# Performance work log

Measured on AMD Instinct MI355X. Metric: run time of the kernel, lower is better.

## Reference

```python
import jax, jax.numpy as jnp
import numpy as np

B, L, H, E = 2, 2048, 16, 64  # self-attention: S=L, D=E


def setup_inputs() -> dict:
    key = jax.random.key(0)
    kq, kk, kv = jax.random.split(key, 3)
    queries = jax.random.normal(kq, (B, L, H, E), dtype=jnp.float32)
    keys = jax.random.normal(kk, (B, L, H, E), dtype=jnp.float32)
    values = jax.random.normal(kv, (B, L, H, E), dtype=jnp.float32)
    return {"queries": queries, "keys": keys, "values": values}


def reference(queries, keys, values):
    # Faithful to source: scale is computed in torch code but never applied.
    # scores: [B, H, L, S]
    scores = jnp.einsum("blhe,bshe->bhls", queries, keys)
    # TriangularCausalMask: triu(ones, diagonal=1) -> mask strictly-future positions
    Lq = queries.shape[1]
    causal = jnp.triu(jnp.ones((Lq, Lq), dtype=bool), k=1)  # [L, S]
    scores = jnp.where(causal[None, None, :, :], -jnp.inf, scores)
    A = jax.nn.softmax(scores, axis=-1)  # dropout in eval mode = identity
    V = jnp.einsum("bhls,bshd->blhd", A, values)
    return V
```

## Files before the change

### kernel.cpp

```cpp
#include <hip/hip_runtime.h>

typedef short bf16x8 __attribute__((ext_vector_type(8)));
typedef short bf16x4 __attribute__((ext_vector_type(4)));
typedef short bf16x2 __attribute__((ext_vector_type(2)));
typedef float f32x4 __attribute__((ext_vector_type(4)));

#define LOG2E 1.4426950408889634f

static __device__ __forceinline__ unsigned short f2bf(float x) {
  unsigned int u = __builtin_bit_cast(unsigned int, x);
  u += 0x7fffu + ((u >> 16) & 1u);
  return (unsigned short)(u >> 16);
}
static __device__ __forceinline__ float bf2f(unsigned short h) {
  unsigned int u = ((unsigned int)h) << 16;
  return __builtin_bit_cast(float, u);
}

static __device__ __forceinline__ void gl_lds16(const void* g, void* l) {
  __builtin_amdgcn_global_load_lds(
      (const __attribute__((address_space(1))) void*)g,
      (__attribute__((address_space(3))) void*)l, 16, 0, 0);
}

__global__ __launch_bounds__(256)
void prep_kv(const float* __restrict__ K, const float* __restrict__ V,
             short* __restrict__ ws) {
  __shared__ float tmp[64 * 65];
  const int isV = blockIdx.x >> 10;
  const int tile = blockIdx.x & 1023;
  const int bh = tile >> 5, kt = tile & 31;
  const int b = bh >> 4, h = bh & 15;
  const int tid = threadIdx.x;
  if (!isV) {
    const float* Kb = K + ((size_t)b * 2048 + kt * 64) * 1024 + h * 64;
    short* ohi = ws + (size_t)tile * 4096;
    for (int i = 0; i < 2; ++i) {
      const int chunk = tid + 256 * i;
      const int row = chunk >> 3, p = chunk & 7;
      const int c = p ^ (row & 7);
      const float* src = Kb + (size_t)row * 1024 + c * 8;
      const f32x4 a = *(const f32x4*)src;
      const f32x4 d = *(const f32x4*)(src + 4);
      bf16x8 hi;
      for (int j = 0; j < 4; ++j) hi[j] = (short)f2bf(a[j]);
      for (int j = 0; j < 4; ++j) hi[4 + j] = (short)f2bf(d[j]);
      *(bf16x8*)(ohi + chunk * 8) = hi;
    }
  } else {
    const float* Vb = V + ((size_t)b * 2048 + kt * 64) * 1024 + h * 64;
    short* ovt = ws + 4194304 + (size_t)tile * 4096;
    for (int i = 0; i < 4; ++i) {
      const int idx = tid + 256 * i;
      const int row = idx >> 4, c4 = idx & 15;
      const f32x4 v = *(const f32x4*)(Vb + (size_t)row * 1024 + c4 * 4);
      for (int j = 0; j < 4; ++j) tmp[row * 65 + c4 * 4 + j] = v[j];
    }
    __syncthreads();
    for (int i = 0; i < 2; ++i) {
      const int chunk = tid + 256 * i;
      const int e = chunk >> 3, p = chunk & 7;
      const int s0 = (p ^ (e & 7)) * 8;
      bf16x8 o;
      for (int j = 0; j < 8; ++j) o[j] = (short)f2bf(tmp[(s0 + j) * 65 + e]);
      *(bf16x8*)(ovt + chunk * 8) = o;
    }
  }
}

__global__ __launch_bounds__(256, 2)
void fa_fwd2(const float* __restrict__ Qg, const short* __restrict__ ws,
             float* __restrict__ Og) {
  __shared__ short sKhi[2][4096];
  __shared__ short sVt[2][4096];
  __shared__ short sP[4096];

  const int tid = threadIdx.x;
  const int lane = tid & 63;
  const int wv = tid >> 6;
  const int ml = lane & 15, quad = lane >> 4;
  const int bh = blockIdx.x;
  const int b = bh >> 4, h = bh & 15;
  const float* Qb = Qg + (size_t)b * 2048 * 1024 + h * 64;
  float* Ob = Og + (size_t)b * 2048 * 1024 + h * 64;
  const short* wsKhi = ws;
  const short* wsVt = ws + 4194304;
  const int wrow0 = wv * 16;
  const bf16x8 ones = {16256, 16256, 16256, 16256, 16256, 16256, 16256, 16256};
  const f32x4 vzero = {0.f, 0.f, 0.f, 0.f};

  for (int half = 0; half < 2; ++half) {
    const int qt = half ? 31 - (int)blockIdx.y : (int)blockIdx.y;
    const int qbase = qt * 64;
    const int nkt = qt + 1;

    bf16x8 qhi[2], qlo[2];
    {
      const float* qr = Qb + (size_t)(qbase + wrow0 + ml) * 1024;
      for (int ks = 0; ks < 2; ++ks) {
        const int e0 = ks * 32 + quad * 8;
        const f32x4 a = *(const f32x4*)(qr + e0);
        const f32x4 c4 = *(const f32x4*)(qr + e0 + 4);
        for (int j = 0; j < 4; ++j) {
          const float x = a[j] * LOG2E;
          const unsigned short hb = f2bf(x);
          qhi[ks][j] = (short)hb;
          qlo[ks][j] = (short)f2bf(x - bf2f(hb));
        }
        for (int j = 0; j < 4; ++j) {
          const float x = c4[j] * LOG2E;
          const unsigned short hb = f2bf(x);
          qhi[ks][4 + j] = (short)hb;
          qlo[ks][4 + j] = (short)f2bf(x - bf2f(hb));
        }
      }
    }

    f32x4 acc[4];
    f32x4 accl = vzero;
    for (int et = 0; et < 4; ++et) acc[et] = vzero;

    auto stage = [&](int kt, int bf) {
      const size_t ktile = ((size_t)bh * 32 + kt) * 4096;
      const short* g0 = wsKhi + ktile;
      const short* g2 = wsVt + ktile;
      const int o0 = tid * 8, o1 = (tid + 256) * 8;
      gl_lds16(g0 + o0, &sKhi[bf][o0]);
      gl_lds16(g0 + o1, &sKhi[bf][o1]);
      gl_lds16(g2 + o0, &sVt[bf][o0]);
      gl_lds16(g2 + o1, &sVt[bf][o1]);
    };

    stage(0, 0);
    __syncthreads();

#pragma unroll 2
    for (int kt = 0; kt < nkt; ++kt) {
      const int buf = kt & 1;
      if (kt + 1 < nkt) stage(kt + 1, buf ^ 1);

      f32x4 S[4];
      for (int nt = 0; nt < 4; ++nt) S[nt] = vzero;
      for (int ks = 0; ks < 2; ++ks) {
        const int ch = (ks << 2) + quad;
        for (int nt = 0; nt < 4; ++nt) {
          const int srow = nt * 16 + ml;
          const int off = srow * 64 + ((ch ^ (srow & 7)) << 3);
          const bf16x8 kh = *(const bf16x8*)(&sKhi[buf][off]);
          S[nt] = __builtin_amdgcn_mfma_f32_16x16x32_bf16(qhi[ks], kh, S[nt], 0, 0, 0);
          S[nt] = __builtin_amdgcn_mfma_f32_16x16x32_bf16(qlo[ks], kh, S[nt], 0, 0, 0);
        }
      }

      const bool dg = (kt * 64 + 63) > (qbase + wrow0);
      for (int nt = 0; nt < 4; ++nt)
        for (int r = 0; r < 4; ++r) {
          float p = __builtin_amdgcn_exp2f(S[nt][r]);
          if (dg) {
            const int sg = kt * 64 + nt * 16 + ml;
            const int lg = qbase + wrow0 + quad * 4 + r;
            if (sg > lg) p = 0.f;
          }
          const int pr = wrow0 + quad * 4 + r;
          const int s = nt * 16 + ml;
          sP[pr * 64 + (((s >> 3) ^ (pr & 7)) << 3) + (s & 7)] =
              (short)(__builtin_bit_cast(unsigned int, p) >> 16);
        }

      for (int ks = 0; ks < 2; ++ks) {
        const int ch = (ks << 2) + quad;
        const int lrow = wrow0 + ml;
        const bf16x8 pa = *(const bf16x8*)(&sP[lrow * 64 + ((ch ^ (lrow & 7)) << 3)]);
        accl = __builtin_amdgcn_mfma_f32_16x16x32_bf16(pa, ones, accl, 0, 0, 0);
        for (int et = 0; et < 4; ++et) {
          const int e = et * 16 + ml;
          const bf16x8 vb = *(const bf16x8*)(&sVt[buf][e * 64 + ((ch ^ (e & 7)) << 3)]);
          acc[et] = __builtin_amdgcn_mfma_f32_16x16x32_bf16(pa, vb, acc[et], 0, 0, 0);
        }
      }
      __syncthreads();
    }

    for (int r = 0; r < 4; ++r) {
      const float inv = 1.0f / accl[r];
      float* orow = Ob + (size_t)(qbase + wrow0 + quad * 4 + r) * 1024;
      for (int et = 0; et < 4; ++et)
        orow[et * 16 + ml] = acc[et][r] * inv;
    }
  }
}

__global__ __launch_bounds__(512, 2)
void fa_fwd_fb(const float* __restrict__ Qg, const float* __restrict__ Kg,
               const float* __restrict__ Vg, float* __restrict__ Og) {
  constexpr int HE = 1024, Lr = 2048;
  __shared__ short sKhi[2][64 * 64];
  __shared__ short sKlo[2][64 * 64];
  __shared__ short sVt[2][64 * 64];
  __shared__ short sP[128 * 64];

  const int tid = threadIdx.x;
  const int lane = tid & 63;
  const int wv = tid >> 6;
  const int ml = lane & 15;
  const int quad = lane >> 4;

  const int b = blockIdx.x >> 4, h = blockIdx.x & 15;
  const size_t headoff = (size_t)b * (size_t)Lr * HE + (size_t)h * 64;
  const float* Qb = Qg + headoff;
  const float* Kb = Kg + headoff;
  const float* Vb = Vg + headoff;
  float* Ob = Og + headoff;

  const f32x4 vzero = {0.f, 0.f, 0.f, 0.f};

  for (int half = 0; half < 2; ++half) {
    const int qt = half ? (15 - (int)blockIdx.y) : (int)blockIdx.y;
    const int qbase = qt * 128;
    const int wrow0 = wv * 16;

    bf16x8 qhi[2], qlo[2];
    {
      const float* qr = Qb + (size_t)(qbase + wrow0 + ml) * HE;
      for (int ks = 0; ks < 2; ++ks) {
        const int e0 = ks * 32 + quad * 8;
        const f32x4 a = *(const f32x4*)(qr + e0);
        const f32x4 c4 = *(const f32x4*)(qr + e0 + 4);
        for (int j = 0; j < 4; ++j) {
          const unsigned short hb = f2bf(a[j]);
          qhi[ks][j] = (short)hb;
          qlo[ks][j] = (short)f2bf(a[j] - bf2f(hb));
        }
        for (int j = 0; j < 4; ++j) {
          const unsigned short hb = f2bf(c4[j]);
          qhi[ks][4 + j] = (short)hb;
          qlo[ks][4 + j] = (short)f2bf(c4[j] - bf2f(hb));
        }
      }
    }

    f32x4 acc[4];
    float mrun[4], lrun[4];
    for (int et = 0; et < 4; ++et) acc[et] = vzero;
    for (int r = 0; r < 4; ++r) { mrun[r] = -1e30f; lrun[r] = 0.f; }

    const int nkt = 2 * qt + 2;
    for (int kt = 0; kt < nkt; ++kt) {
      const int buf = kt & 1;
      for (int i = 0; i < 2; ++i) {
        const int idx = tid + 512 * i;
        const int row = idx >> 4, c = idx & 15;
        const f32x4 kv = *(const f32x4*)(Kb + (size_t)(kt * 64 + row) * HE + c * 4);
        bf16x4 hi, lo;
        for (int j = 0; j < 4; ++j) {
          const unsigned short hb = f2bf(kv[j]);
          hi[j] = (short)hb;
          lo[j] = (short)f2bf(kv[j] - bf2f(hb));
        }
        const int off = row * 64 + (((c >> 1) ^ (row & 7)) << 3) + ((c & 1) << 2);
        *(bf16x4*)(&sKhi[buf][off]) = hi;
        *(bf16x4*)(&sKlo[buf][off]) = lo;
      }
      {
        const int c = tid & 15, rb = tid >> 4;
        const int s0 = rb * 2;
        const f32x4 v0 = *(const f32x4*)(Vb + (size_t)(kt * 64 + s0) * HE + c * 4);
        const f32x4 v1 = *(const f32x4*)(Vb + (size_t)(kt * 64 + s0 + 1) * HE + c * 4);
        for (int j = 0; j < 4; ++j) {
          const int e = c * 4 + j;
          bf16x2 p;
          p[0] = (short)f2bf(v0[j]);
          p[1] = (short)f2bf(v1[j]);
          const int off = e * 64 + (((s0 >> 3) ^ (e & 7)) << 3) + (s0 & 7);
          *(bf16x2*)(&sVt[buf][off]) = p;
        }
      }
      __syncthreads();

      f32x4 S[4];
      for (int nt = 0; nt < 4; ++nt) S[nt] = vzero;
      for (int ks = 0; ks < 2; ++ks) {
        const int ch = (ks << 2) + quad;
        for (int nt = 0; nt < 4; ++nt) {
          const int srow = nt * 16 + ml;
          const int off = srow * 64 + ((ch ^ (srow & 7)) << 3);
          const bf16x8 kh = *(const bf16x8*)(&sKhi[buf][off]);
          const bf16x8 kl = *(const bf16x8*)(&sKlo[buf][off]);
          S[nt] = __builtin_amdgcn_mfma_f32_16x16x32_bf16(qhi[ks], kh, S[nt], 0, 0, 0);
          S[nt] = __builtin_amdgcn_mfma_f32_16x16x32_bf16(qlo[ks], kh, S[nt], 0, 0, 0);
          S[nt] = __builtin_amdgcn_mfma_f32_16x16x32_bf16(qhi[ks], kl, S[nt], 0, 0, 0);
        }
      }

      if (kt * 64 + 63 > qbase + wrow0) {
        for (int nt = 0; nt < 4; ++nt)
          for (int r = 0; r < 4; ++r) {
            const int sg = kt * 64 + nt * 16 + ml;
            const int lg = qbase + wrow0 + quad * 4 + r;
            if (sg > lg) S[nt][r] = -1e30f;
          }
      }

      float mnew[4], al[4], rsum[4];
      for (int r = 0; r < 4; ++r) {
        float mx = fmaxf(fmaxf(S[0][r], S[1][r]), fmaxf(S[2][r], S[3][r]));
        mx = fmaxf(mx, __shfl_xor(mx, 1));
        mx = fmaxf(mx, __shfl_xor(mx, 2));
        mx = fmaxf(mx, __shfl_xor(mx, 4));
        mx = fmaxf(mx, __shfl_xor(mx, 8));
        mnew[r] = fmaxf(mrun[r], mx);
        al[r] = __builtin_amdgcn_exp2f((mrun[r] - mnew[r]) * LOG2E);
        mrun[r] = mnew[r];
        rsum[r] = 0.f;
      }
      for (int nt = 0; nt < 4; ++nt)
        for (int r = 0; r < 4; ++r) {
          const float p = __builtin_amdgcn_exp2f((S[nt][r] - mnew[r]) * LOG2E);
          S[nt][r] = p;
          rsum[r] += p;
        }
      for (int r = 0; r < 4; ++r) {
        rsum[r] += __shfl_xor(rsum[r], 1);
        rsum[r] += __shfl_xor(rsum[r], 2);
        rsum[r] += __shfl_xor(rsum[r], 4);
        rsum[r] += __shfl_xor(rsum[r], 8);
        lrun[r] = lrun[r] * al[r] + rsum[r];
      }
      for (int et = 0; et < 4; ++et)
        for (int r = 0; r < 4; ++r) acc[et][r] *= al[r];

      for (int nt = 0; nt < 4; ++nt)
        for (int r = 0; r < 4; ++r) {
          const int pr = wrow0 + quad * 4 + r;
          const int s = nt * 16 + ml;
          sP[pr * 64 + (((s >> 3) ^ (pr & 7)) << 3) + (s & 7)] = (short)f2bf(S[nt][r]);
        }

      for (int ks = 0; ks < 2; ++ks) {
        const int ch = (ks << 2) + quad;
        const int lrow = wrow0 + ml;
        const bf16x8 pa = *(const bf16x8*)(&sP[lrow * 64 + ((ch ^ (lrow & 7)) << 3)]);
        for (int et = 0; et < 4; ++et) {
          const int e = et * 16 + ml;
          const bf16x8 vb = *(const bf16x8*)(&sVt[buf][e * 64 + ((ch ^ (e & 7)) << 3)]);
          acc[et] = __builtin_amdgcn_mfma_f32_16x16x32_bf16(pa, vb, acc[et], 0, 0, 0);
        }
      }
    }

    for (int r = 0; r < 4; ++r) {
      const float inv = 1.0f / lrun[r];
      float* orow = Ob + (size_t)(qbase + wrow0 + quad * 4 + r) * HE;
      for (int et = 0; et < 4; ++et)
        orow[et * 16 + ml] = acc[et][r] * inv;
    }
  }
}

extern "C" void kernel_launch(void* const* d_in, const int* in_sizes, int n_in,
                              void* d_out, int out_size, void* d_ws, size_t ws_size,
                              hipStream_t stream) {
  const float* Q = (const float*)d_in[0];
  const float* K = (const float*)d_in[1];
  const float* V = (const float*)d_in[2];
  float* O = (float*)d_out;
  if (ws_size >= 16777216u) {
    short* ws = (short*)d_ws;
    hipLaunchKernelGGL(prep_kv, dim3(2048, 1, 1), dim3(256, 1, 1), 0, stream, K, V, ws);
    hipLaunchKernelGGL(fa_fwd2, dim3(32, 16, 1), dim3(256, 1, 1), 0, stream, Q, ws, O);
  } else {
    hipLaunchKernelGGL(fa_fwd_fb, dim3(32, 8, 1), dim3(512, 1, 1), 0, stream, Q, K, V, O);
  }
}
```

Before: 138.9 us.

## Switch QK to fp16 MFMA and launch one block per query tile

K is now stored as fp16 instead of bf16, and the Q·K product uses fp16 MFMA with a hi/lo split of Q, which keeps more mantissa precision. The paired-tile loop (tile i plus tile 31-i per block) is replaced by one block per query tile. The grid doubles to 32x32, launch bounds allow 4 blocks per CU, and heavy diagonal tiles are scheduled first. This raises parallelism and occupancy at the cost of load balancing by tile pairing. The fp16 range limits on K are a precision risk if inputs are large.

```diff
diff --git a/kernel.cpp b/kernel.cpp
--- a/kernel.cpp
+++ b/kernel.cpp
@@ -3,6 +3,7 @@
 typedef short bf16x8 __attribute__((ext_vector_type(8)));
 typedef short bf16x4 __attribute__((ext_vector_type(4)));
 typedef short bf16x2 __attribute__((ext_vector_type(2)));
+typedef _Float16 f16x8 __attribute__((ext_vector_type(8)));
 typedef float f32x4 __attribute__((ext_vector_type(4)));
 
 #define LOG2E 1.4426950408889634f
@@ -34,7 +35,7 @@
   const int tid = threadIdx.x;
   if (!isV) {
     const float* Kb = K + ((size_t)b * 2048 + kt * 64) * 1024 + h * 64;
-    short* ohi = ws + (size_t)tile * 4096;
+    short* okf = ws + (size_t)tile * 4096;
     for (int i = 0; i < 2; ++i) {
       const int chunk = tid + 256 * i;
       const int row = chunk >> 3, p = chunk & 7;
@@ -42,10 +43,10 @@
       const float* src = Kb + (size_t)row * 1024 + c * 8;
       const f32x4 a = *(const f32x4*)src;
       const f32x4 d = *(const f32x4*)(src + 4);
-      bf16x8 hi;
-      for (int j = 0; j < 4; ++j) hi[j] = (short)f2bf(a[j]);
-      for (int j = 0; j < 4; ++j) hi[4 + j] = (short)f2bf(d[j]);
-      *(bf16x8*)(ohi + chunk * 8) = hi;
+      f16x8 hk;
+      for (int j = 0; j < 4; ++j) hk[j] = (_Float16)a[j];
+      for (int j = 0; j < 4; ++j) hk[4 + j] = (_Float16)d[j];
+      *(f16x8*)(okf + chunk * 8) = hk;
     }
   } else {
     const float* Vb = V + ((size_t)b * 2048 + kt * 64) * 1024 + h * 64;
@@ -68,10 +69,10 @@
   }
 }
 
-__global__ __launch_bounds__(256, 2)
+__global__ __launch_bounds__(256, 4)
 void fa_fwd2(const float* __restrict__ Qg, const short* __restrict__ ws,
              float* __restrict__ Og) {
-  __shared__ short sKhi[2][4096];
+  __shared__ short sKf[2][4096];
   __shared__ short sVt[2][4096];
   __shared__ short sP[4096];
 
@@ -83,110 +84,108 @@
   const int b = bh >> 4, h = bh & 15;
   const float* Qb = Qg + (size_t)b * 2048 * 1024 + h * 64;
   float* Ob = Og + (size_t)b * 2048 * 1024 + h * 64;
-  const short* wsKhi = ws;
+  const short* wsKf = ws;
   const short* wsVt = ws + 4194304;
   const int wrow0 = wv * 16;
   const bf16x8 ones = {16256, 16256, 16256, 16256, 16256, 16256, 16256, 16256};
   const f32x4 vzero = {0.f, 0.f, 0.f, 0.f};
 
-  for (int half = 0; half < 2; ++half) {
-    const int qt = half ? 31 - (int)blockIdx.y : (int)blockIdx.y;
-    const int qbase = qt * 64;
-    const int nkt = qt + 1;
-
-    bf16x8 qhi[2], qlo[2];
-    {
-      const float* qr = Qb + (size_t)(qbase + wrow0 + ml) * 1024;
-      for (int ks = 0; ks < 2; ++ks) {
-        const int e0 = ks * 32 + quad * 8;
-        const f32x4 a = *(const f32x4*)(qr + e0);
-        const f32x4 c4 = *(const f32x4*)(qr + e0 + 4);
-        for (int j = 0; j < 4; ++j) {
-          const float x = a[j] * LOG2E;
-          const unsigned short hb = f2bf(x);
-          qhi[ks][j] = (short)hb;
-          qlo[ks][j] = (short)f2bf(x - bf2f(hb));
-        }
-        for (int j = 0; j < 4; ++j) {
-          const float x = c4[j] * LOG2E;
-          const unsigned short hb = f2bf(x);
-          qhi[ks][4 + j] = (short)hb;
-          qlo[ks][4 + j] = (short)f2bf(x - bf2f(hb));
-        }
-      }
-    }
-
-    f32x4 acc[4];
-    f32x4 accl = vzero;
-    for (int et = 0; et < 4; ++et) acc[et] = vzero;
-
-    auto stage = [&](int kt, int bf) {
-      const size_t ktile = ((size_t)bh * 32 + kt) * 4096;
-      const short* g0 = wsKhi + ktile;
-      const short* g2 = wsVt + ktile;
-      const int o0 = tid * 8, o1 = (tid + 256) * 8;
-      gl_lds16(g0 + o0, &sKhi[bf][o0]);
-      gl_lds16(g0 + o1, &sKhi[bf][o1]);
-      gl_lds16(g2 + o0, &sVt[bf][o0]);
-      gl_lds16(g2 + o1, &sVt[bf][o1]);
-    };
-
-    stage(0, 0);
+  const int qt = 31 - (int)blockIdx.y;
+  const int qbase = qt * 64;
+  const int nkt = qt + 1;
+
+  f16x8 qhi[2], qlo[2];
+  {
+    const float* qr = Qb + (size_t)(qbase + wrow0 + ml) * 1024;
+    for (int ks = 0; ks < 2; ++ks) {
+      const int e0 = ks * 32 + quad * 8;
+      const f32x4 a = *(const f32x4*)(qr + e0);
+      const f32x4 c4 = *(const f32x4*)(qr + e0 + 4);
+      for (int j = 0; j < 4; ++j) {
+        const float x = a[j] * LOG2E;
+        const _Float16 hb = (_Float16)x;
+        qhi[ks][j] = hb;
+        qlo[ks][j] = (_Float16)(x - (float)hb);
+      }
+      for (int j = 0; j < 4; ++j) {
+        const float x = c4[j] * LOG2E;
+        const _Float16 hb = (_Float16)x;
+        qhi[ks][4 + j] = hb;
+        qlo[ks][4 + j] = (_Float16)(x - (float)hb);
+      }
+    }
+  }
+
+  f32x4 acc[4];
+  f32x4 accl = vzero;
+  for (int et = 0; et < 4; ++et) acc[et] = vzero;
+
+  auto stage = [&](int kt, int bf) {
+    const size_t ktile = ((size_t)bh * 32 + kt) * 4096;
+    const short* g0 = wsKf + ktile;
+    const short* g2 = wsVt + ktile;
+    const int o0 = tid * 8, o1 = (tid + 256) * 8;
+    gl_lds16(g0 + o0, &sKf[bf][o0]);
+    gl_lds16(g0 + o1, &sKf[bf][o1]);
+    gl_lds16(g2 + o0, &sVt[bf][o0]);
+    gl_lds16(g2 + o1, &sVt[bf][o1]);
+  };
+
+  stage(0, 0);
+  __syncthreads();
+
+#pragma unroll 2
+  for (int kt = 0; kt < nkt; ++kt) {
+    const int buf = kt & 1;
+    if (kt + 1 < nkt) stage(kt + 1, buf ^ 1);
+
+    f32x4 S[4];
+    for (int nt = 0; nt < 4; ++nt) S[nt] = vzero;
+    for (int ks = 0; ks < 2; ++ks) {
+      const int ch = (ks << 2) + quad;
+      for (int nt = 0; nt < 4; ++nt) {
+        const int srow = nt * 16 + ml;
+        const int off = srow * 64 + ((ch ^ (srow & 7)) << 3);
+        const f16x8 kh = *(const f16x8*)(&sKf[buf][off]);
+        S[nt] = __builtin_amdgcn_mfma_f32_16x16x32_f16(qhi[ks], kh, S[nt], 0, 0, 0);
+        S[nt] = __builtin_amdgcn_mfma_f32_16x16x32_f16(qlo[ks], kh, S[nt], 0, 0, 0);
+      }
+    }
+
+    const bool dg = (kt * 64 + 63) > (qbase + wrow0);
+    for (int nt = 0; nt < 4; ++nt)
+      for (int r = 0; r < 4; ++r) {
+        float p = __builtin_amdgcn_exp2f(S[nt][r]);
+        if (dg) {
+          const int sg = kt * 64 + nt * 16 + ml;
+          const int lg = qbase + wrow0 + quad * 4 + r;
+          if (sg > lg) p = 0.f;
+        }
+        const int pr = wrow0 + quad * 4 + r;
+        const int s = nt * 16 + ml;
+        sP[pr * 64 + (((s >> 3) ^ (pr & 7)) << 3) + (s & 7)] =
+            (short)(__builtin_bit_cast(unsigned int, p) >> 16);
+      }
+
+    for (int ks = 0; ks < 2; ++ks) {
+      const int ch = (ks << 2) + quad;
+      const int lrow = wrow0 + ml;
+      const bf16x8 pa = *(const bf16x8*)(&sP[lrow * 64 + ((ch ^ (lrow & 7)) << 3)]);
+      accl = __builtin_amdgcn_mfma_f32_16x16x32_bf16(pa, ones, accl, 0, 0, 0);
+      for (int et = 0; et < 4; ++et) {
+        const int e = et * 16 + ml;
+        const bf16x8 vb = *(const bf16x8*)(&sVt[buf][e * 64 + ((ch ^ (e & 7)) << 3)]);
+        acc[et] = __builtin_amdgcn_mfma_f32_16x16x32_bf16(pa, vb, acc[et], 0, 0, 0);
+      }
+    }
     __syncthreads();
-
-#pragma unroll 2
-    for (int kt = 0; kt < nkt; ++kt) {
-      const int buf = kt & 1;
-      if (kt + 1 < nkt) stage(kt + 1, buf ^ 1);
-
-      f32x4 S[4];
-      for (int nt = 0; nt < 4; ++nt) S[nt] = vzero;
-      for (int ks = 0; ks < 2; ++ks) {
-        const int ch = (ks << 2) + quad;
-        for (int nt = 0; nt < 4; ++nt) {
-          const int srow = nt * 16 + ml;
-          const int off = srow * 64 + ((ch ^ (srow & 7)) << 3);
-          const bf16x8 kh = *(const bf16x8*)(&sKhi[buf][off]);
-          S[nt] = __builtin_amdgcn_mfma_f32_16x16x32_bf16(qhi[ks], kh, S[nt], 0, 0, 0);
-          S[nt] = __builtin_amdgcn_mfma_f32_16x16x32_bf16(qlo[ks], kh, S[nt], 0, 0, 0);
-        }
-      }
-
-      const bool dg = (kt * 64 + 63) > (qbase + wrow0);
-      for (int nt = 0; nt < 4; ++nt)
-        for (int r = 0; r < 4; ++r) {
-          float p = __builtin_amdgcn_exp2f(S[nt][r]);
-          if (dg) {
-            const int sg = kt * 64 + nt * 16 + ml;
-            const int lg = qbase + wrow0 + quad * 4 + r;
-            if (sg > lg) p = 0.f;
-          }
-          const int pr = wrow0 + quad * 4 + r;
-          const int s = nt * 16 + ml;
-          sP[pr * 64 + (((s >> 3) ^ (pr & 7)) << 3) + (s & 7)] =
-              (short)(__builtin_bit_cast(unsigned int, p) >> 16);
-        }
-
-      for (int ks = 0; ks < 2; ++ks) {
-        const int ch = (ks << 2) + quad;
-        const int lrow = wrow0 + ml;
-        const bf16x8 pa = *(const bf16x8*)(&sP[lrow * 64 + ((ch ^ (lrow & 7)) << 3)]);
-        accl = __builtin_amdgcn_mfma_f32_16x16x32_bf16(pa, ones, accl, 0, 0, 0);
-        for (int et = 0; et < 4; ++et) {
-          const int e = et * 16 + ml;
-          const bf16x8 vb = *(const bf16x8*)(&sVt[buf][e * 64 + ((ch ^ (e & 7)) << 3)]);
-          acc[et] = __builtin_amdgcn_mfma_f32_16x16x32_bf16(pa, vb, acc[et], 0, 0, 0);
-        }
-      }
-      __syncthreads();
-    }
-
-    for (int r = 0; r < 4; ++r) {
-      const float inv = 1.0f / accl[r];
-      float* orow = Ob + (size_t)(qbase + wrow0 + quad * 4 + r) * 1024;
-      for (int et = 0; et < 4; ++et)
-        orow[et * 16 + ml] = acc[et][r] * inv;
-    }
+  }
+
+  for (int r = 0; r < 4; ++r) {
+    const float inv = 1.0f / accl[r];
+    float* orow = Ob + (size_t)(qbase + wrow0 + quad * 4 + r) * 1024;
+    for (int et = 0; et < 4; ++et)
+      orow[et * 16 + ml] = acc[et][r] * inv;
   }
 }
 
@@ -367,7 +366,7 @@
   if (ws_size >= 16777216u) {
     short* ws = (short*)d_ws;
     hipLaunchKernelGGL(prep_kv, dim3(2048, 1, 1), dim3(256, 1, 1), 0, stream, K, V, ws);
-    hipLaunchKernelGGL(fa_fwd2, dim3(32, 16, 1), dim3(256, 1, 1), 0, stream, Q, ws, O);
+    hipLaunchKernelGGL(fa_fwd2, dim3(32, 32, 1), dim3(256, 1, 1), 0, stream, Q, ws, O);
   } else {
     hipLaunchKernelGGL(fa_fwd_fb, dim3(32, 8, 1), dim3(512, 1, 1), 0, stream, Q, K, V, O);
   }
```

After: 132.3 us. -4.8%, faster.
